# Performance work log

Measured on AMD Instinct MI355X. Metric: run time of the kernel, lower is better.

## Reference

```python
import jax, jax.numpy as jnp
import numpy as np
import itertools

LN_EPS = 1e-3  # keras LayerNormalization default epsilon

def _pair_indices(field_num):
    pairs = np.array(list(itertools.combinations(range(field_num), 2)), dtype=np.int32)
    return pairs[:, 0], pairs[:, 1]

def setup_inputs() -> dict:
    key = jax.random.key(0)
    ks = jax.random.split(key, 3)
    B, F, E, P, D = 2048, 40, 32, 780, 16
    x = jax.random.normal(ks[0], (B, F, E), dtype=jnp.float32)
    # glorot-normal-ish scaling for the bilinear pair weights
    W = jax.random.normal(ks[1], (P, E, E), dtype=jnp.float32) * (2.0 / (E + E)) ** 0.5
    dense_w = jax.random.normal(ks[2], (P, D), dtype=jnp.float32) * (2.0 / (P + D)) ** 0.5
    dense_b = jnp.zeros((D,), dtype=jnp.float32)
    gamma = jnp.ones((D,), dtype=jnp.float32)
    beta = jnp.zeros((D,), dtype=jnp.float32)
    return {"x": x, "W": W, "dense_w": dense_w, "dense_b": dense_b,
            "gamma": gamma, "beta": beta}

def reference(x, W, dense_w, dense_b, gamma, beta):
    F = x.shape[1]
    idx_i, idx_j = _pair_indices(F)           # static pair lists, P = C(F,2)
    xi = x[:, idx_i, :]                        # [B, P, E]
    xj = x[:, idx_j, :]                        # [B, P, E]
    # (x_i @ W_p) . x_j per pair, fused: p[b,p] = sum_ef xi[b,p,e] W[p,e,f] xj[b,p,f]
    t = jnp.einsum('bpe,pef->bpf', xi, W)      # [B, P, E]
    p = jnp.einsum('bpf,bpf->bp', t, xj)       # [B, P]
    # reducing layer: Dense(output_dim) + LayerNorm (no activation)
    h = p @ dense_w + dense_b                  # [B, D]
    mu = jnp.mean(h, axis=-1, keepdims=True)
    var = jnp.mean(jnp.square(h - mu), axis=-1, keepdims=True)
    out = (h - mu) * jax.lax.rsqrt(var + LN_EPS) * gamma + beta
    return out
```

## Files before the change

kernel.cpp:

```cpp
#include <hip/hip_runtime.h>
#include <hip/hip_bf16.h>

typedef __attribute__((ext_vector_type(8))) short bf16x8;
typedef __attribute__((ext_vector_type(4))) float f32x4;

#define B_NUM 2048
#define F_NUM 40
#define E_DIM 32
#define P_NUM 780
#define D_DIM 16
#define PC_N  65
#define PC_SZ 12
#define LN_EPS 1e-3f

#define WF_OFF 0
#define WF_BYTES (P_NUM * 2 * 64 * 8 * 2)
#define XB_OFF  WF_BYTES
#define XB_BYTES (F_NUM * 4 * B_NUM * 8 * 2)
#define DW_OFF  (XB_OFF + XB_BYTES)
#define DW_BYTES 32768
#define HP_OFF  (DW_OFF + DW_BYTES)

static __device__ __forceinline__ unsigned short f2b(float f) {
  unsigned u = __builtin_bit_cast(unsigned, f);
  u += 0x7fffu + ((u >> 16) & 1u);
  return (unsigned short)(u >> 16);
}
static __device__ __forceinline__ short f2bs(float f) { return (short)f2b(f); }
static __device__ __forceinline__ short fcvt(float f) {
  return (short)__bfloat16_as_ushort(__float2bfloat16(f));
}
static __device__ __forceinline__ float b2f(unsigned short u) {
  return __builtin_bit_cast(float, (unsigned)u << 16);
}

__global__ __launch_bounds__(256) void prep_kernel(
    const float* __restrict__ x, const float* __restrict__ W,
    const float* __restrict__ dw, short* __restrict__ xbp,
    short* __restrict__ wfrag, unsigned short* __restrict__ dwbf) {
  const int lane = threadIdx.x & 63;
  const int wv   = threadIdx.x >> 6;
  const int lhi = lane >> 4, llo = lane & 15;
  __shared__ float wst[4][E_DIM * E_DIM];

  if (blockIdx.x < 640) {
    const int u  = blockIdx.x * 256 + threadIdx.x;
    const int b  = u & (B_NUM - 1);
    const int fp = u >> 11;
    const int f  = fp >> 1;
    const float* src = x + ((size_t)b * F_NUM + f) * E_DIM + (fp & 1) * 16;
    const float4 v0 = *reinterpret_cast<const float4*>(src);
    const float4 v1 = *reinterpret_cast<const float4*>(src + 4);
    const float4 v2 = *reinterpret_cast<const float4*>(src + 8);
    const float4 v3 = *reinterpret_cast<const float4*>(src + 12);
    const int plane = f * 4 + (fp & 1) * 2;
    bf16x8 o0, o1;
    o0[0] = f2bs(v0.x); o0[1] = f2bs(v0.y); o0[2] = f2bs(v0.z); o0[3] = f2bs(v0.w);
    o0[4] = f2bs(v1.x); o0[5] = f2bs(v1.y); o0[6] = f2bs(v1.z); o0[7] = f2bs(v1.w);
    o1[0] = f2bs(v2.x); o1[1] = f2bs(v2.y); o1[2] = f2bs(v2.z); o1[3] = f2bs(v2.w);
    o1[4] = f2bs(v3.x); o1[5] = f2bs(v3.y); o1[6] = f2bs(v3.z); o1[7] = f2bs(v3.w);
    *reinterpret_cast<bf16x8*>(xbp + ((size_t)plane * B_NUM + b) * 8)       = o0;
    *reinterpret_cast<bf16x8*>(xbp + ((size_t)(plane + 1) * B_NUM + b) * 8) = o1;
  } else if (blockIdx.x < 640 + 195) {
    const int p = (blockIdx.x - 640) * 4 + wv;
    const float* Wp = W + (size_t)p * (E_DIM * E_DIM);
#pragma unroll
    for (int k = 0; k < 4; ++k) {
      float4 v = *reinterpret_cast<const float4*>(Wp + k * 256 + lane * 4);
      *reinterpret_cast<float4*>(&wst[wv][k * 256 + lane * 4]) = v;
    }
#pragma unroll
    for (int frag = 0; frag < 2; ++frag) {
      const int fo = (llo >> 2) * 8 + frag * 4 + (llo & 3);
      bf16x8 v;
#pragma unroll
      for (int t = 0; t < 8; ++t)
        v[t] = f2bs(wst[wv][(lhi * 8 + t) * E_DIM + fo]);
      *reinterpret_cast<bf16x8*>(wfrag + ((size_t)(p * 2 + frag) * 64 + lane) * 8) = v;
    }
  } else {
    for (int t = threadIdx.x; t < P_NUM * D_DIM; t += 256) dwbf[t] = f2b(dw[t]);
  }
}

__global__ __launch_bounds__(256, 2) void fused_bilinear_dense_kernel(
    const short* __restrict__ xbp, const short* __restrict__ wfrag,
    const unsigned short* __restrict__ dwbf, float* __restrict__ hpart) {
  const int lane = threadIdx.x & 63;
  const int wv   = threadIdx.x >> 6;
  const int lhi = lane >> 4, llo = lane & 15;
  const int bb = blockIdx.x * 256 + wv * 64;
  const int pc = blockIdx.y;
  const int p0 = pc * PC_SZ;

  int off[4];
#pragma unroll
  for (int nt = 0; nt < 4; ++nt)
    off[nt] = (lhi * B_NUM + bb + nt * 16 + llo) * 8;
#define XB8(f, o) (*reinterpret_cast<const bf16x8*>(xbp + (size_t)(f) * 65536 + (o)))
#define AFR(p, fr) (*reinterpret_cast<const bf16x8*>( \
    wfrag + ((size_t)((p) * 2 + (fr)) * 64 + lane) * 8))

  int ii[PC_SZ], jj[PC_SZ];
  {
    int i = 0;
    while ((i + 1) * (79 - (i + 1)) / 2 <= p0) ++i;
    ii[0] = i; jj[0] = i + 1 + (p0 - i * (79 - i) / 2);
  }
#pragma unroll
  for (int k = 1; k < PC_SZ; ++k) {
    int in_ = ii[k - 1], jn = jj[k - 1] + 1;
    if (jn == F_NUM) { ++in_; jn = in_ + 1; }
    ii[k] = in_; jj[k] = jn;
  }

  bf16x8 bf[4];
#pragma unroll
  for (int nt = 0; nt < 4; ++nt) bf[nt] = XB8(ii[0], off[nt]);

  bf16x8 sxj[2][4], sa0[2], sa1[2];
  unsigned short sdw[2];
#pragma unroll
  for (int s = 0; s < 2; ++s) {
#pragma unroll
    for (int nt = 0; nt < 4; ++nt) sxj[s][nt] = XB8(jj[s], off[nt]);
    sa0[s] = AFR(p0 + s, 0);
    sa1[s] = AFR(p0 + s, 1);
    sdw[s] = dwbf[(p0 + s) * D_DIM + llo];
  }

  f32x4 acc[4];
#pragma unroll
  for (int nt = 0; nt < 4; ++nt) acc[nt] = {0.f, 0.f, 0.f, 0.f};
  const f32x4 z = {0.f, 0.f, 0.f, 0.f};

#pragma unroll
  for (int k = 0; k < PC_SZ; ++k) {
    const int s = k & 1;
    const bf16x8 a0 = sa0[s], a1 = sa1[s];
    const bf16x8 xj0 = sxj[s][0], xj1 = sxj[s][1];
    const bf16x8 xj2 = sxj[s][2], xj3 = sxj[s][3];
    const unsigned short dwb = sdw[s];
    if (k + 2 < PC_SZ) {
#pragma unroll
      for (int nt = 0; nt < 4; ++nt) sxj[s][nt] = XB8(jj[k + 2], off[nt]);
      sa0[s] = AFR(p0 + k + 2, 0);
      sa1[s] = AFR(p0 + k + 2, 1);
      sdw[s] = dwbf[(p0 + k + 2) * D_DIM + llo];
    }

    __builtin_amdgcn_s_setprio(1);
    f32x4 c0[4], c1[4];
#pragma unroll
    for (int nt = 0; nt < 4; ++nt) {
      c0[nt] = __builtin_amdgcn_mfma_f32_16x16x32_bf16(a0, bf[nt], z, 0, 0, 0);
      c1[nt] = __builtin_amdgcn_mfma_f32_16x16x32_bf16(a1, bf[nt], z, 0, 0, 0);
    }

    bf16x8 a2;
#pragma unroll
    for (int t = 0; t < 8; ++t) a2[t] = (short)dwb;

    const bf16x8 xjl[4] = {xj0, xj1, xj2, xj3};
#pragma unroll
    for (int nt = 0; nt < 4; ++nt) {
      bf16x8 u;
#pragma unroll
      for (int t = 0; t < 4; ++t) {
        u[t]     = fcvt(c0[nt][t] * b2f((unsigned short)xjl[nt][t]));
        u[t + 4] = fcvt(c1[nt][t] * b2f((unsigned short)xjl[nt][t + 4]));
      }
      acc[nt] = __builtin_amdgcn_mfma_f32_16x16x32_bf16(a2, u, acc[nt], 0, 0, 0);
    }
    __builtin_amdgcn_s_setprio(0);

    if (k + 1 < PC_SZ && ii[k + 1] != ii[k]) {
#pragma unroll
      for (int nt = 0; nt < 4; ++nt) bf[nt] = XB8(ii[k + 1], off[nt]);
    }
  }
#undef XB8
#undef AFR

  float* hp = hpart + (size_t)pc * B_NUM * D_DIM;
#pragma unroll
  for (int nt = 0; nt < 4; ++nt)
    *reinterpret_cast<f32x4*>(hp + (size_t)(bb + nt * 16 + llo) * D_DIM + lhi * 4) = acc[nt];
}

__global__ __launch_bounds__(256) void reduce_ln_kernel(
    const float* __restrict__ hpart, const float* __restrict__ bias,
    const float* __restrict__ gamma, const float* __restrict__ beta,
    float* __restrict__ out) {
  const int t = threadIdx.x;
  const int d = t & 15;
  const int b = blockIdx.x * 16 + (t >> 4);
  float acc = bias[d];
  const float* hp = hpart + (size_t)b * D_DIM + d;
#pragma unroll 5
  for (int pc = 0; pc < PC_N; ++pc)
    acc += hp[(size_t)pc * B_NUM * D_DIM];

  float sum = acc;
  sum += __shfl_xor(sum, 1); sum += __shfl_xor(sum, 2);
  sum += __shfl_xor(sum, 4); sum += __shfl_xor(sum, 8);
  const float mu = sum * (1.f / D_DIM);
  const float dev = acc - mu;
  float v = dev * dev;
  v += __shfl_xor(v, 1); v += __shfl_xor(v, 2);
  v += __shfl_xor(v, 4); v += __shfl_xor(v, 8);
  const float rs = rsqrtf(v * (1.f / D_DIM) + LN_EPS);
  out[(size_t)b * D_DIM + d] = dev * rs * gamma[d] + beta[d];
}

extern "C" void kernel_launch(void* const* d_in, const int* in_sizes, int n_in,
                              void* d_out, int out_size, void* d_ws, size_t ws_size,
                              hipStream_t stream) {
  const float* x     = (const float*)d_in[0];
  const float* W     = (const float*)d_in[1];
  const float* dw    = (const float*)d_in[2];
  const float* db    = (const float*)d_in[3];
  const float* gamma = (const float*)d_in[4];
  const float* beta  = (const float*)d_in[5];
  float* out = (float*)d_out;

  short*          wfrag = (short*)((char*)d_ws + WF_OFF);
  short*          xbp   = (short*)((char*)d_ws + XB_OFF);
  unsigned short* dwbf  = (unsigned short*)((char*)d_ws + DW_OFF);
  float*          hpart = (float*)((char*)d_ws + HP_OFF);

  prep_kernel<<<640 + 195 + 1, 256, 0, stream>>>(x, W, dw, xbp, wfrag, dwbf);

  dim3 gA(B_NUM / 256, PC_N);
  fused_bilinear_dense_kernel<<<gA, 256, 0, stream>>>(xbp, wfrag, dwbf, hpart);

  reduce_ln_kernel<<<B_NUM / 16, 256, 0, stream>>>(hpart, db, gamma, beta, out);
}
```

Baseline: 34.15 us.

## Fuse W and dense-weight bf16 conversion into main kernel via shared memory

Removes the W-fragment and dense-weight preprocessing from the prep kernel. Each main-kernel block now loads its 12 fp32 W matrices, converts them to bf16 in shared memory and rearranges them into MFMA A-fragments read from LDS. Dense weights are read as fp32 and converted in the loop. This drops a global round-trip for W, but the conversion is repeated across the 8 batch blocks of each pair chunk and adds two barriers plus LDS use that may lower occupancy. The reduce loop unroll is also raised.

```diff
diff --git a/kernel.cpp b/kernel.cpp
--- a/kernel.cpp
+++ b/kernel.cpp
@@ -3,6 +3,7 @@
 
 typedef __attribute__((ext_vector_type(8))) short bf16x8;
 typedef __attribute__((ext_vector_type(4))) float f32x4;
+typedef __attribute__((ext_vector_type(4))) unsigned short u16x4;
 
 #define B_NUM 2048
 #define F_NUM 40
@@ -13,13 +14,9 @@
 #define PC_SZ 12
 #define LN_EPS 1e-3f
 
-#define WF_OFF 0
-#define WF_BYTES (P_NUM * 2 * 64 * 8 * 2)
-#define XB_OFF  WF_BYTES
+#define XB_OFF  0
 #define XB_BYTES (F_NUM * 4 * B_NUM * 8 * 2)
-#define DW_OFF  (XB_OFF + XB_BYTES)
-#define DW_BYTES 32768
-#define HP_OFF  (DW_OFF + DW_BYTES)
+#define HP_OFF  XB_BYTES
 
 static __device__ __forceinline__ unsigned short f2b(float f) {
   unsigned u = __builtin_bit_cast(unsigned, f);
@@ -34,72 +31,72 @@
   return __builtin_bit_cast(float, (unsigned)u << 16);
 }
 
-__global__ __launch_bounds__(256) void prep_kernel(
-    const float* __restrict__ x, const float* __restrict__ W,
-    const float* __restrict__ dw, short* __restrict__ xbp,
-    short* __restrict__ wfrag, unsigned short* __restrict__ dwbf) {
-  const int lane = threadIdx.x & 63;
-  const int wv   = threadIdx.x >> 6;
-  const int lhi = lane >> 4, llo = lane & 15;
-  __shared__ float wst[4][E_DIM * E_DIM];
-
-  if (blockIdx.x < 640) {
-    const int u  = blockIdx.x * 256 + threadIdx.x;
-    const int b  = u & (B_NUM - 1);
-    const int fp = u >> 11;
-    const int f  = fp >> 1;
-    const float* src = x + ((size_t)b * F_NUM + f) * E_DIM + (fp & 1) * 16;
-    const float4 v0 = *reinterpret_cast<const float4*>(src);
-    const float4 v1 = *reinterpret_cast<const float4*>(src + 4);
-    const float4 v2 = *reinterpret_cast<const float4*>(src + 8);
-    const float4 v3 = *reinterpret_cast<const float4*>(src + 12);
-    const int plane = f * 4 + (fp & 1) * 2;
-    bf16x8 o0, o1;
-    o0[0] = f2bs(v0.x); o0[1] = f2bs(v0.y); o0[2] = f2bs(v0.z); o0[3] = f2bs(v0.w);
-    o0[4] = f2bs(v1.x); o0[5] = f2bs(v1.y); o0[6] = f2bs(v1.z); o0[7] = f2bs(v1.w);
-    o1[0] = f2bs(v2.x); o1[1] = f2bs(v2.y); o1[2] = f2bs(v2.z); o1[3] = f2bs(v2.w);
-    o1[4] = f2bs(v3.x); o1[5] = f2bs(v3.y); o1[6] = f2bs(v3.z); o1[7] = f2bs(v3.w);
-    *reinterpret_cast<bf16x8*>(xbp + ((size_t)plane * B_NUM + b) * 8)       = o0;
-    *reinterpret_cast<bf16x8*>(xbp + ((size_t)(plane + 1) * B_NUM + b) * 8) = o1;
-  } else if (blockIdx.x < 640 + 195) {
-    const int p = (blockIdx.x - 640) * 4 + wv;
-    const float* Wp = W + (size_t)p * (E_DIM * E_DIM);
-#pragma unroll
-    for (int k = 0; k < 4; ++k) {
-      float4 v = *reinterpret_cast<const float4*>(Wp + k * 256 + lane * 4);
-      *reinterpret_cast<float4*>(&wst[wv][k * 256 + lane * 4]) = v;
-    }
-#pragma unroll
-    for (int frag = 0; frag < 2; ++frag) {
-      const int fo = (llo >> 2) * 8 + frag * 4 + (llo & 3);
-      bf16x8 v;
-#pragma unroll
-      for (int t = 0; t < 8; ++t)
-        v[t] = f2bs(wst[wv][(lhi * 8 + t) * E_DIM + fo]);
-      *reinterpret_cast<bf16x8*>(wfrag + ((size_t)(p * 2 + frag) * 64 + lane) * 8) = v;
-    }
-  } else {
-    for (int t = threadIdx.x; t < P_NUM * D_DIM; t += 256) dwbf[t] = f2b(dw[t]);
-  }
+__global__ __launch_bounds__(256) void xpack_kernel(
+    const float* __restrict__ x, short* __restrict__ xbp) {
+  const int u  = blockIdx.x * 256 + threadIdx.x;
+  const int b  = u & (B_NUM - 1);
+  const int fp = u >> 11;
+  const int f  = fp >> 1;
+  const float* src = x + ((size_t)b * F_NUM + f) * E_DIM + (fp & 1) * 16;
+  const float4 v0 = *reinterpret_cast<const float4*>(src);
+  const float4 v1 = *reinterpret_cast<const float4*>(src + 4);
+  const float4 v2 = *reinterpret_cast<const float4*>(src + 8);
+  const float4 v3 = *reinterpret_cast<const float4*>(src + 12);
+  const int plane = f * 4 + (fp & 1) * 2;
+  bf16x8 o0, o1;
+  o0[0] = f2bs(v0.x); o0[1] = f2bs(v0.y); o0[2] = f2bs(v0.z); o0[3] = f2bs(v0.w);
+  o0[4] = f2bs(v1.x); o0[5] = f2bs(v1.y); o0[6] = f2bs(v1.z); o0[7] = f2bs(v1.w);
+  o1[0] = f2bs(v2.x); o1[1] = f2bs(v2.y); o1[2] = f2bs(v2.z); o1[3] = f2bs(v2.w);
+  o1[4] = f2bs(v3.x); o1[5] = f2bs(v3.y); o1[6] = f2bs(v3.z); o1[7] = f2bs(v3.w);
+  *reinterpret_cast<bf16x8*>(xbp + ((size_t)plane * B_NUM + b) * 8)       = o0;
+  *reinterpret_cast<bf16x8*>(xbp + ((size_t)(plane + 1) * B_NUM + b) * 8) = o1;
 }
 
 __global__ __launch_bounds__(256, 2) void fused_bilinear_dense_kernel(
-    const short* __restrict__ xbp, const short* __restrict__ wfrag,
-    const unsigned short* __restrict__ dwbf, float* __restrict__ hpart) {
-  const int lane = threadIdx.x & 63;
-  const int wv   = threadIdx.x >> 6;
+    const float* __restrict__ W, const float* __restrict__ dw,
+    const short* __restrict__ xbp, float* __restrict__ hpart) {
+  __shared__ unsigned short wraw[PC_SZ * 1024];
+  __shared__ __align__(16) unsigned short afrag[PC_SZ * 2 * 512];
+  const int tid  = threadIdx.x;
+  const int lane = tid & 63, wv = tid >> 6;
   const int lhi = lane >> 4, llo = lane & 15;
   const int bb = blockIdx.x * 256 + wv * 64;
   const int pc = blockIdx.y;
   const int p0 = pc * PC_SZ;
 
+  {
+    const float* Wsrc = W + (size_t)p0 * 1024;
+#pragma unroll
+    for (int it = 0; it < PC_SZ; ++it) {
+      const int L = it * 1024 + tid * 4;
+      float4 v = *reinterpret_cast<const float4*>(Wsrc + L);
+      u16x4 o;
+      o[0] = f2b(v.x); o[1] = f2b(v.y); o[2] = f2b(v.z); o[3] = f2b(v.w);
+      *reinterpret_cast<u16x4*>(&wraw[L]) = o;
+    }
+  }
+  __syncthreads();
+
+#pragma unroll
+  for (int s = 0; s < 3; ++s) {
+    const int pl = wv * 3 + s;
+#pragma unroll
+    for (int frag = 0; frag < 2; ++frag) {
+      const int fo = (llo >> 2) * 8 + frag * 4 + (llo & 3);
+      bf16x8 v;
+#pragma unroll
+      for (int t = 0; t < 8; ++t)
+        v[t] = (short)wraw[pl * 1024 + (lhi * 8 + t) * E_DIM + fo];
+      *reinterpret_cast<bf16x8*>(&afrag[(pl * 2 + frag) * 512 + lane * 8]) = v;
+    }
+  }
+  __syncthreads();
+
   int off[4];
 #pragma unroll
   for (int nt = 0; nt < 4; ++nt)
     off[nt] = (lhi * B_NUM + bb + nt * 16 + llo) * 8;
 #define XB8(f, o) (*reinterpret_cast<const bf16x8*>(xbp + (size_t)(f) * 65536 + (o)))
-#define AFR(p, fr) (*reinterpret_cast<const bf16x8*>( \
-    wfrag + ((size_t)((p) * 2 + (fr)) * 64 + lane) * 8))
 
   int ii[PC_SZ], jj[PC_SZ];
   {
@@ -118,15 +115,13 @@
 #pragma unroll
   for (int nt = 0; nt < 4; ++nt) bf[nt] = XB8(ii[0], off[nt]);
 
-  bf16x8 sxj[2][4], sa0[2], sa1[2];
-  unsigned short sdw[2];
+  bf16x8 sxj[2][4];
+  float sdwf[2];
 #pragma unroll
   for (int s = 0; s < 2; ++s) {
 #pragma unroll
     for (int nt = 0; nt < 4; ++nt) sxj[s][nt] = XB8(jj[s], off[nt]);
-    sa0[s] = AFR(p0 + s, 0);
-    sa1[s] = AFR(p0 + s, 1);
-    sdw[s] = dwbf[(p0 + s) * D_DIM + llo];
+    sdwf[s] = dw[(p0 + s) * D_DIM + llo];
   }
 
   f32x4 acc[4];
@@ -137,17 +132,17 @@
 #pragma unroll
   for (int k = 0; k < PC_SZ; ++k) {
     const int s = k & 1;
-    const bf16x8 a0 = sa0[s], a1 = sa1[s];
     const bf16x8 xj0 = sxj[s][0], xj1 = sxj[s][1];
     const bf16x8 xj2 = sxj[s][2], xj3 = sxj[s][3];
-    const unsigned short dwb = sdw[s];
+    const float dwf = sdwf[s];
     if (k + 2 < PC_SZ) {
 #pragma unroll
       for (int nt = 0; nt < 4; ++nt) sxj[s][nt] = XB8(jj[k + 2], off[nt]);
-      sa0[s] = AFR(p0 + k + 2, 0);
-      sa1[s] = AFR(p0 + k + 2, 1);
-      sdw[s] = dwbf[(p0 + k + 2) * D_DIM + llo];
-    }
+      sdwf[s] = dw[(p0 + k + 2) * D_DIM + llo];
+    }
+
+    const bf16x8 a0 = *reinterpret_cast<const bf16x8*>(&afrag[(k * 2 + 0) * 512 + lane * 8]);
+    const bf16x8 a1 = *reinterpret_cast<const bf16x8*>(&afrag[(k * 2 + 1) * 512 + lane * 8]);
 
     __builtin_amdgcn_s_setprio(1);
     f32x4 c0[4], c1[4];
@@ -157,9 +152,10 @@
       c1[nt] = __builtin_amdgcn_mfma_f32_16x16x32_bf16(a1, bf[nt], z, 0, 0, 0);
     }
 
+    const short dwb = fcvt(dwf);
     bf16x8 a2;
 #pragma unroll
-    for (int t = 0; t < 8; ++t) a2[t] = (short)dwb;
+    for (int t = 0; t < 8; ++t) a2[t] = dwb;
 
     const bf16x8 xjl[4] = {xj0, xj1, xj2, xj3};
 #pragma unroll
@@ -180,7 +176,6 @@
     }
   }
 #undef XB8
-#undef AFR
 
   float* hp = hpart + (size_t)pc * B_NUM * D_DIM;
 #pragma unroll
@@ -197,7 +192,7 @@
   const int b = blockIdx.x * 16 + (t >> 4);
   float acc = bias[d];
   const float* hp = hpart + (size_t)b * D_DIM + d;
-#pragma unroll 5
+#pragma unroll 13
   for (int pc = 0; pc < PC_N; ++pc)
     acc += hp[(size_t)pc * B_NUM * D_DIM];
 
@@ -224,15 +219,13 @@
   const float* beta  = (const float*)d_in[5];
   float* out = (float*)d_out;
 
-  short*          wfrag = (short*)((char*)d_ws + WF_OFF);
-  short*          xbp   = (short*)((char*)d_ws + XB_OFF);
-  unsigned short* dwbf  = (unsigned short*)((char*)d_ws + DW_OFF);
-  float*          hpart = (float*)((char*)d_ws + HP_OFF);
-
-  prep_kernel<<<640 + 195 + 1, 256, 0, stream>>>(x, W, dw, xbp, wfrag, dwbf);
+  short* xbp   = (short*)((char*)d_ws + XB_OFF);
+  float* hpart = (float*)((char*)d_ws + HP_OFF);
+
+  xpack_kernel<<<640, 256, 0, stream>>>(x, xbp);
 
   dim3 gA(B_NUM / 256, PC_N);
-  fused_bilinear_dense_kernel<<<gA, 256, 0, stream>>>(xbp, wfrag, dwbf, hpart);
+  fused_bilinear_dense_kernel<<<gA, 256, 0, stream>>>(W, dw, xbp, hpart);
 
   reduce_ln_kernel<<<B_NUM / 16, 256, 0, stream>>>(hpart, db, gamma, beta, out);
 }
```

After: 30.91 us. -9.5%, faster.
